# Optimization experiments

Hardware: AMD Instinct MI355X
Metric: run time of the kernel (lower is better)

The kernel has to match this reference:

```python
import jax, jax.numpy as jnp
import numpy as np

B, S, D = 4, 4096, 64

def setup_inputs() -> dict:
    key = jax.random.key(0)
    ks = jax.random.split(key, 6)
    mk = lambda k: jax.random.normal(k, (B, S, D), dtype=jnp.float32)
    return {
        "q_re": mk(ks[0]), "q_im": mk(ks[1]),
        "k_re": mk(ks[2]), "k_im": mk(ks[3]),
        "v_re": mk(ks[4]), "v_im": mk(ks[5]),
    }

def reference(q_re, q_im, k_re, k_im, v_re, v_im):
    # Complex QK^T (no conjugate, matching torch.bmm on complex tensors):
    # (qr + i qi)(kr + i ki)^T -> re = qr kr^T - qi ki^T ; im = qr ki^T + qi kr^T
    d_k = q_re.shape[-1]
    scale = 1.0 / jnp.sqrt(jnp.asarray(d_k, dtype=q_re.dtype))
    s_re = (jnp.einsum('bqd,bkd->bqk', q_re, k_re)
            - jnp.einsum('bqd,bkd->bqk', q_im, k_im)) * scale
    s_im = (jnp.einsum('bqd,bkd->bqk', q_re, k_im)
            + jnp.einsum('bqd,bkd->bqk', q_im, k_re)) * scale
    # softmax over |scores| along key axis; weights are real (imag part is 0)
    w = jax.nn.softmax(jnp.sqrt(s_re * s_re + s_im * s_im), axis=-1)  # [B,S,S]
    # CVDropout is identity in eval mode. Output = real_weights @ complex_values
    o_re = jnp.einsum('bqk,bkd->bqd', w, v_re)
    o_im = jnp.einsum('bqk,bkd->bqd', w, v_im)
    return jnp.stack([o_re, o_im], axis=0)  # [2, B, S, D] (real, imag)
```

## Files before the change

kernel.cpp:

```cpp
#include <hip/hip_runtime.h>
#include <stdint.h>

#define B_    4
#define S_    4096
#define D_    64
#define QBLK  64
#define KVBLK 64
#define NT    (S_ / KVBLK)
#define NELEM (B_ * S_ * D_)

typedef __attribute__((ext_vector_type(8))) short bf16x8;
typedef __attribute__((ext_vector_type(4))) short bf16x4;
typedef __attribute__((ext_vector_type(4))) float f32x4;
typedef __attribute__((ext_vector_type(4))) int   i32x4;
typedef __attribute__((ext_vector_type(4))) unsigned u32x4;

#define MFMA(a, b, c) __builtin_amdgcn_mfma_f32_16x16x32_bf16(a, b, c, 0, 0, 0)
#define VMWAIT(n) asm volatile("s_waitcnt vmcnt(" #n ")" ::: "memory")
#define BARRIER() do { asm volatile("" ::: "memory"); __builtin_amdgcn_s_barrier(); asm volatile("" ::: "memory"); } while (0)
#define LGKM_FENCE() do { asm volatile("s_waitcnt lgkmcnt(0)" ::: "memory"); __builtin_amdgcn_sched_barrier(0); } while (0)

__device__ __forceinline__ short f2bf(float x) {
    unsigned u = __builtin_bit_cast(unsigned, x);
    u += 0x7FFFu + ((u >> 16) & 1u);
    return (short)(u >> 16);
}

__device__ __forceinline__ unsigned cvtpk(float lo, float hi) {
    unsigned r;
    asm("v_cvt_pk_bf16_f32 %0, %1, %2" : "=v"(r) : "v"(lo), "v"(hi));
    return r;
}

__device__ __forceinline__ void async16(const short* g, short* l) {
    __builtin_amdgcn_global_load_lds(
        (const __attribute__((address_space(1))) unsigned int*)g,
        (__attribute__((address_space(3))) unsigned int*)l, 16, 0, 0);
}

__global__ __launch_bounds__(256)
void cvt4_kernel(const float* __restrict__ a0, const float* __restrict__ a1,
                 const float* __restrict__ a2, const float* __restrict__ a3,
                 short* __restrict__ ws) {
    const int idx = blockIdx.x * 256 + threadIdx.x;
    const int tn  = idx >> 18;
    const int e4  = idx & ((1 << 18) - 1);
    const float* s = (tn == 0 ? a0 : tn == 1 ? a1 : tn == 2 ? a2 : a3) + (size_t)e4 * 4;
    const float sc = (tn < 2) ? 0.125f : 1.0f;
    f32x4 x = *(const f32x4*)s;
    bf16x4 v;
#pragma unroll
    for (int c = 0; c < 4; ++c) v[c] = f2bf(x[c] * sc);
    *(bf16x4*)(ws + (size_t)tn * NELEM + (size_t)e4 * 4) = v;
}

__global__ __launch_bounds__(256)
void transpose_v_kernel(const float* __restrict__ v_re, const float* __restrict__ v_im,
                        short* __restrict__ vrT, short* __restrict__ viT) {
    __shared__ short tile[64][72];
    const int tid  = threadIdx.x;
    const int sb   = blockIdx.x;
    const int b    = blockIdx.y;
    const int comp = blockIdx.z;
    const float* src = comp ? v_im : v_re;
    short*       dst = comp ? viT : vrT;
#pragma unroll
    for (int i = 0; i < 4; ++i) {
        const int slot = i * 256 + tid;
        const int s  = slot >> 4;
        const int d4 = slot & 15;
        f32x4 x = *(const f32x4*)(src + (((size_t)b * S_) + sb * 64 + s) * D_ + d4 * 4);
#pragma unroll
        for (int c = 0; c < 4; ++c) tile[d4 * 4 + c][s] = f2bf(x[c]);
    }
    __syncthreads();
#pragma unroll
    for (int i = 0; i < 2; ++i) {
        const int slot = i * 256 + tid;
        const int d  = slot >> 3;
        const int c8 = slot & 7;
        bf16x8 v;
#pragma unroll
        for (int j = 0; j < 8; ++j) v[j] = tile[d][c8 * 8 + j];
        *(bf16x8*)(dst + ((size_t)b * 64 + d) * S_ + sb * 64 + c8 * 8) = v;
    }
}

template<int SPLIT>
__global__ __launch_bounds__(256, 4)
void cv_attn_main(const short* __restrict__ wsb,
                  float* __restrict__ out,
                  float* __restrict__ opart,
                  float* __restrict__ ml)
{
    __shared__ __align__(16) short smem[4 * KVBLK * D_];
    short* kr_s = smem;
    short* ki_s = smem + 4096;
    short* vr_s = smem + 8192;
    short* vi_s = smem + 12288;

    const int tid  = threadIdx.x;
    const int lane = tid & 63;
    const int wv   = tid >> 6;
    const int l15  = lane & 15;
    const int h    = lane >> 4;

    int bid = blockIdx.x;
    const int nwg = B_ * 64 * SPLIT;
    bid = (bid & 7) * (nwg >> 3) + (bid >> 3);
    const int qb = bid & 63;
    const int sp = (bid >> 6) % SPLIT;
    const int b  = bid / (64 * SPLIT);

    const short* qr  = wsb;
    const short* qi  = wsb + (size_t)NELEM;
    const short* kr  = wsb + 2 * (size_t)NELEM;
    const short* ki  = wsb + 3 * (size_t)NELEM;
    const short* vrT = wsb + 4 * (size_t)NELEM;
    const short* viT = wsb + 5 * (size_t)NELEM;

    const int qrow = qb * QBLK + wv * 16 + l15;
    const size_t qoff = ((size_t)b * S_ + qrow) * D_;
    bf16x8 fqr[2], fqi[2], fqn[2];
#pragma unroll
    for (int dh = 0; dh < 2; ++dh) {
        fqr[dh] = *(const bf16x8*)(qr + qoff + dh * 32 + h * 8);
        fqi[dh] = *(const bf16x8*)(qi + qoff + dh * 32 + h * 8);
        i32x4 n = __builtin_bit_cast(i32x4, fqi[dh]) ^ (int)0x80008000;
        fqn[dh] = __builtin_bit_cast(bf16x8, n);
    }

    f32x4 o_re[4], o_im[4];
#pragma unroll
    for (int i = 0; i < 4; ++i) {
        o_re[i] = (f32x4){0.f, 0.f, 0.f, 0.f};
        o_im[i] = (f32x4){0.f, 0.f, 0.f, 0.f};
    }
    float m_run = -1e30f, l_run = 0.f;
    const float L2E = 1.44269504088896f;

    const int r8   = lane >> 3;
    const int u16l = lane & 7;
    constexpr int TPB = NT / SPLIT;

    auto stageK = [&](int t) {
        const int kb = (sp * TPB + t) * KVBLK;
#pragma unroll
        for (int i = 0; i < 2; ++i) {
            const int row   = wv * 16 + i * 8 + r8;
            const int lbase = (wv * 16 + i * 8) * 64;
            const int swz   = (u16l ^ (row & 7)) << 3;
            const size_t koff = ((size_t)b * S_ + kb + row) * 64 + swz;
            async16(kr + koff, kr_s + lbase);
            async16(ki + koff, ki_s + lbase);
        }
    };
    auto stageV = [&](int t) {
        const int kb = (sp * TPB + t) * KVBLK;
#pragma unroll
        for (int i = 0; i < 2; ++i) {
            const int row   = wv * 16 + i * 8 + r8;
            const int lbase = (wv * 16 + i * 8) * 64;
            const int swz   = (u16l ^ (row & 7)) << 3;
            const size_t voff = ((size_t)b * 64 + row) * S_ + kb + swz;
            async16(vrT + voff, vr_s + lbase);
            async16(viT + voff, vi_s + lbase);
        }
    };

    stageK(0);
    stageV(0);

    for (int tt = 0; tt < TPB; ++tt) {
        const bool last = (tt == TPB - 1);

        VMWAIT(4);
        BARRIER();

        f32x4 s_re[4], s_im[4];
#pragma unroll
        for (int c = 0; c < 4; ++c) {
            s_re[c] = (f32x4){0.f, 0.f, 0.f, 0.f};
            s_im[c] = (f32x4){0.f, 0.f, 0.f, 0.f};
        }
        __builtin_amdgcn_s_setprio(1);
#pragma unroll
        for (int c = 0; c < 4; ++c) {
            const int krow = c * 16 + l15;
#pragma unroll
            for (int dh = 0; dh < 2; ++dh) {
                const int u = ((dh * 4 + h) ^ (krow & 7)) << 3;
                bf16x8 fkr = *(const bf16x8*)(kr_s + krow * 64 + u);
                bf16x8 fki = *(const bf16x8*)(ki_s + krow * 64 + u);
                s_re[c] = MFMA(fkr, fqr[dh], s_re[c]);
                s_re[c] = MFMA(fki, fqn[dh], s_re[c]);
                s_im[c] = MFMA(fki, fqr[dh], s_im[c]);
                s_im[c] = MFMA(fkr, fqi[dh], s_im[c]);
            }
        }
        __builtin_amdgcn_s_setprio(0);

        LGKM_FENCE();
        BARRIER();
        if (!last) stageK(tt + 1);

#pragma unroll
        for (int c = 0; c < 4; ++c) {
            f32x4 g = s_re[c] * s_re[c] + s_im[c] * s_im[c];
#pragma unroll
            for (int r = 0; r < 4; ++r) s_re[c][r] = __builtin_amdgcn_sqrtf(g[r]);
        }
        float tmax = s_re[0][0];
#pragma unroll
        for (int c = 0; c < 4; ++c)
#pragma unroll
            for (int r = 0; r < 4; ++r) tmax = fmaxf(tmax, s_re[c][r]);
        tmax = fmaxf(tmax, __shfl_xor(tmax, 16));
        tmax = fmaxf(tmax, __shfl_xor(tmax, 32));

        if (__any(tmax > m_run + 8.0f)) {
            const float m_new = fmaxf(m_run, tmax);
            const float alpha = __builtin_amdgcn_exp2f((m_run - m_new) * L2E);
            l_run *= alpha;
#pragma unroll
            for (int i = 0; i < 4; ++i) { o_re[i] *= alpha; o_im[i] *= alpha; }
            m_run = m_new;
        }
        const float nm = -m_run * L2E;

#pragma unroll
        for (int c = 0; c < 4; ++c)
#pragma unroll
            for (int r = 0; r < 4; ++r)
                s_im[c][r] = __builtin_amdgcn_exp2f(__builtin_fmaf(s_re[c][r], L2E, nm));
        f32x4 ps = s_im[0] + s_im[1] + s_im[2] + s_im[3];
        l_run += (ps[0] + ps[1]) + (ps[2] + ps[3]);

        bf16x8 pb[2];
#pragma unroll
        for (int hf = 0; hf < 2; ++hf) {
            u32x4 w;
            w[0] = cvtpk(s_im[hf * 2][0],     s_im[hf * 2][1]);
            w[1] = cvtpk(s_im[hf * 2][2],     s_im[hf * 2][3]);
            w[2] = cvtpk(s_im[hf * 2 + 1][0], s_im[hf * 2 + 1][1]);
            w[3] = cvtpk(s_im[hf * 2 + 1][2], s_im[hf * 2 + 1][3]);
            pb[hf] = __builtin_bit_cast(bf16x8, w);
        }

        if (!last) { VMWAIT(4); } else { VMWAIT(0); }
        BARRIER();

        __builtin_amdgcn_s_setprio(1);
#pragma unroll
        for (int hf = 0; hf < 2; ++hf) {
#pragma unroll
            for (int dc = 0; dc < 4; ++dc) {
                const int d  = dc * 16 + l15;
                const int s0 = (((hf * 4 +     (h >> 1)) ^ (l15 & 7)) << 3) + ((h & 1) << 2);
                const int s1 = (((hf * 4 + 2 + (h >> 1)) ^ (l15 & 7)) << 3) + ((h & 1) << 2);
                bf16x4 r0 = *(const bf16x4*)(vr_s + d * 64 + s0);
                bf16x4 r1 = *(const bf16x4*)(vr_s + d * 64 + s1);
                bf16x4 i0 = *(const bf16x4*)(vi_s + d * 64 + s0);
                bf16x4 i1 = *(const bf16x4*)(vi_s + d * 64 + s1);
                bf16x8 av, ai;
#pragma unroll
                for (int j = 0; j < 4; ++j) {
                    av[j] = r0[j]; av[j + 4] = r1[j];
                    ai[j] = i0[j]; ai[j + 4] = i1[j];
                }
                o_re[dc] = MFMA(av, pb[hf], o_re[dc]);
                o_im[dc] = MFMA(ai, pb[hf], o_im[dc]);
            }
        }
        __builtin_amdgcn_s_setprio(0);

        LGKM_FENCE();
        BARRIER();
        if (!last) stageV(tt + 1);
    }

    float lt = l_run;
    lt += __shfl_xor(lt, 16);
    lt += __shfl_xor(lt, 32);
    const float inv = (SPLIT == 1) ? (1.0f / lt) : 1.0f;

    float* ol = (float*)smem;

    float* dst_re;
    float* dst_im;
    if constexpr (SPLIT == 1) {
        dst_re = out + ((size_t)b * S_ + qb * QBLK) * D_;
        dst_im = dst_re + (size_t)NELEM;
    } else {
        const size_t qo = ((size_t)b * S_ + qb * QBLK) * D_;
        dst_re = opart + ((size_t)sp * 2 + 0) * NELEM + qo;
        dst_im = opart + ((size_t)sp * 2 + 1) * NELEM + qo;
    }

    auto store_comp = [&](const f32x4 (&oc)[4], float* og) {
        __syncthreads();
#pragma unroll
        for (int dc = 0; dc < 4; ++dc)
#pragma unroll
            for (int r = 0; r < 4; ++r)
                ol[(wv * 16 + l15) * 65 + dc * 16 + h * 4 + r] = oc[dc][r] * inv;
        __syncthreads();
#pragma unroll
        for (int i = 0; i < 4; ++i) {
            const int slot = i * 256 + tid;
            const int row  = slot >> 4;
            const int c4   = slot & 15;
            f32x4 v;
#pragma unroll
            for (int j = 0; j < 4; ++j) v[j] = ol[row * 65 + c4 * 4 + j];
            *(f32x4*)(og + (size_t)row * D_ + c4 * 4) = v;
        }
    };
    store_comp(o_re, dst_re);
    store_comp(o_im, dst_im);

    if constexpr (SPLIT > 1) {
        if (lane < 16) {
            const int row = qb * QBLK + wv * 16 + lane;
            const size_t mo = ((size_t)sp * (B_ * S_) + (size_t)b * S_ + row) * 2;
            ml[mo]     = m_run;
            ml[mo + 1] = lt;
        }
    }
}

template<int SPLIT>
__global__ __launch_bounds__(256)
void cv_attn_combine(const float* __restrict__ opart, const float* __restrict__ ml,
                     float* __restrict__ out) {
    const int idx  = blockIdx.x * 256 + threadIdx.x;
    const int d4   = idx & 15;
    const int rest = idx >> 4;
    const int row  = rest & (B_ * S_ - 1);
    const int comp = rest >> 14;
    float ms[SPLIT], ls[SPLIT];
    float M = -1e30f;
#pragma unroll
    for (int s = 0; s < SPLIT; ++s) {
        ms[s] = ml[((size_t)s * (B_ * S_) + row) * 2];
        ls[s] = ml[((size_t)s * (B_ * S_) + row) * 2 + 1];
        M = fmaxf(M, ms[s]);
    }
    float L = 0.f;
    f32x4 acc = (f32x4){0.f, 0.f, 0.f, 0.f};
#pragma unroll
    for (int s = 0; s < SPLIT; ++s) {
        const float w = __builtin_amdgcn_exp2f((ms[s] - M) * 1.44269504088896f);
        L += ls[s] * w;
        f32x4 o = *(const f32x4*)(opart + ((size_t)(s * 2 + comp)) * NELEM
                                  + (size_t)row * D_ + d4 * 4);
        acc += o * w;
    }
    const float invL = 1.0f / L;
    acc *= invL;
    *(f32x4*)(out + (size_t)comp * NELEM + (size_t)row * D_ + d4 * 4) = acc;
}

__global__ __launch_bounds__(256, 1)
void cv_attn_legacy(const float* __restrict__ q_re, const float* __restrict__ q_im,
                    const float* __restrict__ k_re, const float* __restrict__ k_im,
                    const float* __restrict__ v_re, const float* __restrict__ v_im,
                    float* __restrict__ out)
{
    __shared__ __align__(16) short smem[4 * KVBLK * D_];
    short* kr_s = smem;
    short* ki_s = smem + 4096;
    short* vr_s = smem + 8192;
    short* vi_s = smem + 12288;

    const int tid  = threadIdx.x;
    const int lane = tid & 63;
    const int wv   = tid >> 6;
    const int l15  = lane & 15;
    const int h    = lane >> 4;

    const int b  = blockIdx.x >> 6;
    const int qb = blockIdx.x & 63;
    const size_t boff = (size_t)b * S_ * D_;

    const int qrow = qb * QBLK + wv * 16 + l15;
    const float* qrp = q_re + boff + (size_t)qrow * D_;
    const float* qip = q_im + boff + (size_t)qrow * D_;
    bf16x8 fqr[2], fqi[2], fqn[2];
#pragma unroll
    for (int dh = 0; dh < 2; ++dh) {
        const int d0 = dh * 32 + h * 8;
        f32x4 a0 = *(const f32x4*)(qrp + d0);
        f32x4 a1 = *(const f32x4*)(qrp + d0 + 4);
        f32x4 b0 = *(const f32x4*)(qip + d0);
        f32x4 b1 = *(const f32x4*)(qip + d0 + 4);
#pragma unroll
        for (int j = 0; j < 4; ++j) {
            fqr[dh][j] = f2bf(a0[j]); fqr[dh][j + 4] = f2bf(a1[j]);
            fqi[dh][j] = f2bf(b0[j]); fqi[dh][j + 4] = f2bf(b1[j]);
            fqn[dh][j] = f2bf(-b0[j]); fqn[dh][j + 4] = f2bf(-b1[j]);
        }
    }

    f32x4 o_re[4], o_im[4];
#pragma unroll
    for (int i = 0; i < 4; ++i) {
        o_re[i] = (f32x4){0.f, 0.f, 0.f, 0.f};
        o_im[i] = (f32x4){0.f, 0.f, 0.f, 0.f};
    }
    float m_run = -1e30f, l_run = 0.f;
    const float SC = 0.125f * 1.44269504088896f;

    for (int t = 0; t < NT; ++t) {
        const int kb = t * KVBLK;
#pragma unroll
        for (int a = 0; a < 2; ++a) {
            const float* src = (a ? k_im : k_re) + boff;
            short* dst = a ? ki_s : kr_s;
#pragma unroll
            for (int i = 0; i < 2; ++i) {
                const int slot = i * 256 + tid;
                const int row  = slot >> 3;
                const int cb   = slot & 7;
                const float* p = src + (size_t)(kb + row) * D_ + cb * 8;
                f32x4 x0 = *(const f32x4*)p;
                f32x4 x1 = *(const f32x4*)(p + 4);
                bf16x8 v;
#pragma unroll
                for (int j = 0; j < 4; ++j) { v[j] = f2bf(x0[j]); v[j + 4] = f2bf(x1[j]); }
                *(bf16x8*)(dst + row * 64 + ((cb ^ (row & 7)) << 3)) = v;
            }
        }
#pragma unroll
        for (int a = 0; a < 2; ++a) {
            const float* src = (a ? v_im : v_re) + boff;
            short* dst = a ? vi_s : vr_s;
#pragma unroll
            for (int i = 0; i < 4; ++i) {
                const int slot = i * 256 + tid;
                const int k  = slot >> 4;
                const int d4 = slot & 15;
                f32x4 x = *(const f32x4*)(src + (size_t)(kb + k) * D_ + d4 * 4);
#pragma unroll
                for (int c = 0; c < 4; ++c) {
                    const int d = d4 * 4 + c;
                    dst[d * 64 + (((k >> 2) ^ (d & 15)) << 2) + (k & 3)] = f2bf(x[c]);
                }
            }
        }
        __syncthreads();

        f32x4 s_re[4], s_im[4];
#pragma unroll
        for (int c = 0; c < 4; ++c) {
            s_re[c] = (f32x4){0.f, 0.f, 0.f, 0.f};
            s_im[c] = (f32x4){0.f, 0.f, 0.f, 0.f};
        }
#pragma unroll
        for (int c = 0; c < 4; ++c) {
            const int krow = c * 16 + l15;
#pragma unroll
            for (int dh = 0; dh < 2; ++dh) {
                const int u = ((dh * 4 + h) ^ (krow & 7)) << 3;
                bf16x8 fkr = *(const bf16x8*)(kr_s + krow * 64 + u);
                bf16x8 fki = *(const bf16x8*)(ki_s + krow * 64 + u);
                s_re[c] = MFMA(fkr, fqr[dh], s_re[c]);
                s_re[c] = MFMA(fki, fqn[dh], s_re[c]);
                s_im[c] = MFMA(fki, fqr[dh], s_im[c]);
                s_im[c] = MFMA(fkr, fqi[dh], s_im[c]);
            }
        }

        float pv[4][4];
        float tmax = 0.f;
#pragma unroll
        for (int c = 0; c < 4; ++c)
#pragma unroll
            for (int r = 0; r < 4; ++r) {
                const float re = s_re[c][r], im = s_im[c][r];
                const float mg = __builtin_amdgcn_sqrtf(re * re + im * im) * SC;
                pv[c][r] = mg;
                tmax = fmaxf(tmax, mg);
            }
        tmax = fmaxf(tmax, __shfl_xor(tmax, 16));
        tmax = fmaxf(tmax, __shfl_xor(tmax, 32));
        const float m_new = fmaxf(m_run, tmax);
        const float alpha = __builtin_amdgcn_exp2f(m_run - m_new);
        m_run = m_new;
        float psum = 0.f;
#pragma unroll
        for (int c = 0; c < 4; ++c)
#pragma unroll
            for (int r = 0; r < 4; ++r) {
                const float e = __builtin_amdgcn_exp2f(pv[c][r] - m_new);
                pv[c][r] = e;
                psum += e;
            }
        l_run = l_run * alpha + psum;
#pragma unroll
        for (int i = 0; i < 4; ++i) { o_re[i] *= alpha; o_im[i] *= alpha; }

        bf16x8 pb[2];
#pragma unroll
        for (int hf = 0; hf < 2; ++hf)
#pragma unroll
            for (int j = 0; j < 4; ++j) {
                pb[hf][j]     = f2bf(pv[hf * 2][j]);
                pb[hf][j + 4] = f2bf(pv[hf * 2 + 1][j]);
            }

#pragma unroll
        for (int hf = 0; hf < 2; ++hf) {
#pragma unroll
            for (int dc = 0; dc < 4; ++dc) {
                const int d  = dc * 16 + l15;
                const int s0 = (((hf * 8) + h)     ^ l15) << 2;
                const int s1 = (((hf * 8) + 4 + h) ^ l15) << 2;
                bf16x4 r0 = *(const bf16x4*)(vr_s + d * 64 + s0);
                bf16x4 r1 = *(const bf16x4*)(vr_s + d * 64 + s1);
                bf16x4 i0 = *(const bf16x4*)(vi_s + d * 64 + s0);
                bf16x4 i1 = *(const bf16x4*)(vi_s + d * 64 + s1);
                bf16x8 av, ai;
#pragma unroll
                for (int j = 0; j < 4; ++j) {
                    av[j] = r0[j]; av[j + 4] = r1[j];
                    ai[j] = i0[j]; ai[j + 4] = i1[j];
                }
                o_re[dc] = MFMA(av, pb[hf], o_re[dc]);
                o_im[dc] = MFMA(ai, pb[hf], o_im[dc]);
            }
        }
        __syncthreads();
    }

    float lt = l_run;
    lt += __shfl_xor(lt, 16);
    lt += __shfl_xor(lt, 32);
    const float inv = 1.0f / lt;

    float* ol = (float*)smem;
    auto store_comp = [&](const f32x4 (&oc)[4], float* og) {
#pragma unroll
        for (int dc = 0; dc < 4; ++dc)
#pragma unroll
            for (int r = 0; r < 4; ++r)
                ol[(wv * 16 + l15) * 65 + dc * 16 + h * 4 + r] = oc[dc][r] * inv;
        __syncthreads();
#pragma unroll
        for (int i = 0; i < 4; ++i) {
            const int slot = i * 256 + tid;
            const int row  = slot >> 4;
            const int c4   = slot & 15;
            f32x4 v;
#pragma unroll
            for (int j = 0; j < 4; ++j) v[j] = ol[row * 65 + c4 * 4 + j];
            *(f32x4*)(og + (size_t)row * D_ + c4 * 4) = v;
        }
        __syncthreads();
    };

    float* og0 = out + boff + (size_t)(qb * QBLK) * D_;
    store_comp(o_re, og0);
    store_comp(o_im, og0 + (size_t)B_ * S_ * D_);
}

extern "C" void kernel_launch(void* const* d_in, const int* in_sizes, int n_in,
                              void* d_out, int out_size, void* d_ws, size_t ws_size,
                              hipStream_t stream) {
    (void)in_sizes; (void)n_in; (void)out_size;
    const float* q_re = (const float*)d_in[0];
    const float* q_im = (const float*)d_in[1];
    const float* k_re = (const float*)d_in[2];
    const float* k_im = (const float*)d_in[3];
    const float* v_re = (const float*)d_in[4];
    const float* v_im = (const float*)d_in[5];
    float* out = (float*)d_out;

    const size_t bf_bytes = 6 * (size_t)NELEM * 2;
    const size_t part4    = 4 * 2 * (size_t)NELEM * 4;
    const size_t ml4      = 4 * (size_t)(B_ * S_) * 2 * 4;
    const size_t need4    = bf_bytes + part4 + ml4;

    if (ws_size >= bf_bytes) {
        short* wsb = (short*)d_ws;
        cvt4_kernel<<<4096, 256, 0, stream>>>(q_re, q_im, k_re, k_im, wsb);
        transpose_v_kernel<<<dim3(64, B_, 2), 256, 0, stream>>>(
            v_re, v_im, wsb + 4 * (size_t)NELEM, wsb + 5 * (size_t)NELEM);
        if (ws_size >= need4) {
            float* opart = (float*)((char*)d_ws + bf_bytes);
            float* ml    = opart + 4 * 2 * (size_t)NELEM;
            cv_attn_main<4><<<B_ * 64 * 4, 256, 0, stream>>>(wsb, nullptr, opart, ml);
            cv_attn_combine<4><<<2048, 256, 0, stream>>>(opart, ml, out);
        } else {
            cv_attn_main<1><<<B_ * 64, 256, 0, stream>>>(wsb, out, nullptr, nullptr);
        }
    } else {
        cv_attn_legacy<<<B_ * 64, 256, 0, stream>>>(q_re, q_im, k_re, k_im, v_re, v_im, out);
    }
}
```

Measured before the change: 87.85 us.

## Merge prepass kernels, permute V layout for vector LDS reads, raise KV split to 8

```diff
diff --git a/kernel.cpp b/kernel.cpp
--- a/kernel.cpp
+++ b/kernel.cpp
@@ -8,12 +8,14 @@
 #define KVBLK 64
 #define NT    (S_ / KVBLK)
 #define NELEM (B_ * S_ * D_)
+#define BS_   (B_ * S_)
 
 typedef __attribute__((ext_vector_type(8))) short bf16x8;
 typedef __attribute__((ext_vector_type(4))) short bf16x4;
 typedef __attribute__((ext_vector_type(4))) float f32x4;
 typedef __attribute__((ext_vector_type(4))) int   i32x4;
 typedef __attribute__((ext_vector_type(4))) unsigned u32x4;
+typedef __attribute__((ext_vector_type(4))) _Float16 f16x4;
 
 #define MFMA(a, b, c) __builtin_amdgcn_mfma_f32_16x16x32_bf16(a, b, c, 0, 0, 0)
 #define VMWAIT(n) asm volatile("s_waitcnt vmcnt(" #n ")" ::: "memory")
@@ -39,58 +41,62 @@
 }
 
 __global__ __launch_bounds__(256)
-void cvt4_kernel(const float* __restrict__ a0, const float* __restrict__ a1,
-                 const float* __restrict__ a2, const float* __restrict__ a3,
-                 short* __restrict__ ws) {
-    const int idx = blockIdx.x * 256 + threadIdx.x;
-    const int tn  = idx >> 18;
-    const int e4  = idx & ((1 << 18) - 1);
-    const float* s = (tn == 0 ? a0 : tn == 1 ? a1 : tn == 2 ? a2 : a3) + (size_t)e4 * 4;
-    const float sc = (tn < 2) ? 0.125f : 1.0f;
-    f32x4 x = *(const f32x4*)s;
-    bf16x4 v;
-#pragma unroll
-    for (int c = 0; c < 4; ++c) v[c] = f2bf(x[c] * sc);
-    *(bf16x4*)(ws + (size_t)tn * NELEM + (size_t)e4 * 4) = v;
-}
-
-__global__ __launch_bounds__(256)
-void transpose_v_kernel(const float* __restrict__ v_re, const float* __restrict__ v_im,
-                        short* __restrict__ vrT, short* __restrict__ viT) {
-    __shared__ short tile[64][72];
+void prepass_kernel(const float* __restrict__ q_re, const float* __restrict__ q_im,
+                    const float* __restrict__ k_re, const float* __restrict__ k_im,
+                    const float* __restrict__ v_re, const float* __restrict__ v_im,
+                    short* __restrict__ ws) {
+    const int bidx = blockIdx.x;
     const int tid  = threadIdx.x;
-    const int sb   = blockIdx.x;
-    const int b    = blockIdx.y;
-    const int comp = blockIdx.z;
-    const float* src = comp ? v_im : v_re;
-    short*       dst = comp ? viT : vrT;
-#pragma unroll
-    for (int i = 0; i < 4; ++i) {
-        const int slot = i * 256 + tid;
-        const int s  = slot >> 4;
-        const int d4 = slot & 15;
-        f32x4 x = *(const f32x4*)(src + (((size_t)b * S_) + sb * 64 + s) * D_ + d4 * 4);
-#pragma unroll
-        for (int c = 0; c < 4; ++c) tile[d4 * 4 + c][s] = f2bf(x[c]);
-    }
-    __syncthreads();
-#pragma unroll
-    for (int i = 0; i < 2; ++i) {
-        const int slot = i * 256 + tid;
-        const int d  = slot >> 3;
-        const int c8 = slot & 7;
-        bf16x8 v;
-#pragma unroll
-        for (int j = 0; j < 8; ++j) v[j] = tile[d][c8 * 8 + j];
-        *(bf16x8*)(dst + ((size_t)b * 64 + d) * S_ + sb * 64 + c8 * 8) = v;
-    }
-}
-
-template<int SPLIT>
+    if (bidx < 4096) {
+        const int idx = bidx * 256 + tid;
+        const int tn  = idx >> 18;
+        const int e4  = idx & ((1 << 18) - 1);
+        const float* s = (tn == 0 ? q_re : tn == 1 ? q_im : tn == 2 ? k_re : k_im)
+                         + (size_t)e4 * 4;
+        const float sc = (tn < 2) ? 0.125f : 1.0f;
+        f32x4 x = *(const f32x4*)s;
+        bf16x4 v;
+#pragma unroll
+        for (int c = 0; c < 4; ++c) v[c] = f2bf(x[c] * sc);
+        *(bf16x4*)(ws + (size_t)tn * NELEM + (size_t)e4 * 4) = v;
+    } else {
+        __shared__ short tile[64][72];
+        const int tb   = bidx - 4096;
+        const int sb   = tb & 63;
+        const int b    = (tb >> 6) & 3;
+        const int comp = tb >> 8;
+        const float* src = comp ? v_im : v_re;
+        short* dst = ws + (size_t)(4 + comp) * NELEM;
+#pragma unroll
+        for (int i = 0; i < 4; ++i) {
+            const int slot = i * 256 + tid;
+            const int s  = slot >> 4;
+            const int d4 = slot & 15;
+            f32x4 x = *(const f32x4*)(src + (((size_t)b * S_) + sb * 64 + s) * D_ + d4 * 4);
+#pragma unroll
+            for (int c = 0; c < 4; ++c) tile[d4 * 4 + c][s] = f2bf(x[c]);
+        }
+        __syncthreads();
+#pragma unroll
+        for (int i = 0; i < 2; ++i) {
+            const int slot = i * 256 + tid;
+            const int d = slot >> 3;
+            const int m = slot & 7;
+            const int a = m >> 2, hh = m & 3;
+            bf16x8 v;
+#pragma unroll
+            for (int j = 0; j < 8; ++j)
+                v[j] = tile[d][a * 32 + hh * 4 + ((j >> 2) << 4) + (j & 3)];
+            *(bf16x8*)(dst + ((size_t)b * 64 + d) * S_ + sb * 64 + m * 8) = v;
+        }
+    }
+}
+
+template<int SPLIT, typename OT>
 __global__ __launch_bounds__(256, 4)
 void cv_attn_main(const short* __restrict__ wsb,
                   float* __restrict__ out,
-                  float* __restrict__ opart,
+                  OT* __restrict__ opart,
                   float* __restrict__ ml)
 {
     __shared__ __align__(16) short smem[4 * KVBLK * D_];
@@ -119,6 +125,9 @@
     const short* vrT = wsb + 4 * (size_t)NELEM;
     const short* viT = wsb + 5 * (size_t)NELEM;
 
+    short* kb0 = smem + l15 * 64 + ((h ^ (l15 & 7)) << 3);
+    short* kb1 = smem + l15 * 64 + (((h ^ 4) ^ (l15 & 7)) << 3);
+
     const int qrow = qb * QBLK + wv * 16 + l15;
     const size_t qoff = ((size_t)b * S_ + qrow) * D_;
     bf16x8 fqr[2], fqi[2], fqn[2];
@@ -186,17 +195,18 @@
         __builtin_amdgcn_s_setprio(1);
 #pragma unroll
         for (int c = 0; c < 4; ++c) {
-            const int krow = c * 16 + l15;
-#pragma unroll
-            for (int dh = 0; dh < 2; ++dh) {
-                const int u = ((dh * 4 + h) ^ (krow & 7)) << 3;
-                bf16x8 fkr = *(const bf16x8*)(kr_s + krow * 64 + u);
-                bf16x8 fki = *(const bf16x8*)(ki_s + krow * 64 + u);
-                s_re[c] = MFMA(fkr, fqr[dh], s_re[c]);
-                s_re[c] = MFMA(fki, fqn[dh], s_re[c]);
-                s_im[c] = MFMA(fki, fqr[dh], s_im[c]);
-                s_im[c] = MFMA(fkr, fqi[dh], s_im[c]);
-            }
+            bf16x8 fkr0 = *(const bf16x8*)(kb0 + c * 1024);
+            bf16x8 fkr1 = *(const bf16x8*)(kb1 + c * 1024);
+            bf16x8 fki0 = *(const bf16x8*)(kb0 + 4096 + c * 1024);
+            bf16x8 fki1 = *(const bf16x8*)(kb1 + 4096 + c * 1024);
+            s_re[c] = MFMA(fkr0, fqr[0], s_re[c]);
+            s_re[c] = MFMA(fkr1, fqr[1], s_re[c]);
+            s_re[c] = MFMA(fki0, fqn[0], s_re[c]);
+            s_re[c] = MFMA(fki1, fqn[1], s_re[c]);
+            s_im[c] = MFMA(fki0, fqr[0], s_im[c]);
+            s_im[c] = MFMA(fki1, fqr[1], s_im[c]);
+            s_im[c] = MFMA(fkr0, fqi[0], s_im[c]);
+            s_im[c] = MFMA(fkr1, fqi[1], s_im[c]);
         }
         __builtin_amdgcn_s_setprio(0);
 
@@ -253,21 +263,11 @@
         __builtin_amdgcn_s_setprio(1);
 #pragma unroll
         for (int hf = 0; hf < 2; ++hf) {
+            const short* kbh = hf ? kb1 : kb0;
 #pragma unroll
             for (int dc = 0; dc < 4; ++dc) {
-                const int d  = dc * 16 + l15;
-                const int s0 = (((hf * 4 +     (h >> 1)) ^ (l15 & 7)) << 3) + ((h & 1) << 2);
-                const int s1 = (((hf * 4 + 2 + (h >> 1)) ^ (l15 & 7)) << 3) + ((h & 1) << 2);
-                bf16x4 r0 = *(const bf16x4*)(vr_s + d * 64 + s0);
-                bf16x4 r1 = *(const bf16x4*)(vr_s + d * 64 + s1);
-                bf16x4 i0 = *(const bf16x4*)(vi_s + d * 64 + s0);
-                bf16x4 i1 = *(const bf16x4*)(vi_s + d * 64 + s1);
-                bf16x8 av, ai;
-#pragma unroll
-                for (int j = 0; j < 4; ++j) {
-                    av[j] = r0[j]; av[j + 4] = r1[j];
-                    ai[j] = i0[j]; ai[j + 4] = i1[j];
-                }
+                bf16x8 av = *(const bf16x8*)(kbh + 8192  + dc * 1024);
+                bf16x8 ai = *(const bf16x8*)(kbh + 12288 + dc * 1024);
                 o_re[dc] = MFMA(av, pb[hf], o_re[dc]);
                 o_im[dc] = MFMA(ai, pb[hf], o_im[dc]);
             }
@@ -286,10 +286,10 @@
 
     float* ol = (float*)smem;
 
-    float* dst_re;
-    float* dst_im;
+    OT* dst_re;
+    OT* dst_im;
     if constexpr (SPLIT == 1) {
-        dst_re = out + ((size_t)b * S_ + qb * QBLK) * D_;
+        dst_re = (OT*)out + ((size_t)b * S_ + qb * QBLK) * D_;
         dst_im = dst_re + (size_t)NELEM;
     } else {
         const size_t qo = ((size_t)b * S_ + qb * QBLK) * D_;
@@ -297,7 +297,7 @@
         dst_im = opart + ((size_t)sp * 2 + 1) * NELEM + qo;
     }
 
-    auto store_comp = [&](const f32x4 (&oc)[4], float* og) {
+    auto store_comp = [&](const f32x4 (&oc)[4], OT* og) {
         __syncthreads();
 #pragma unroll
         for (int dc = 0; dc < 4; ++dc)
@@ -313,7 +313,14 @@
             f32x4 v;
 #pragma unroll
             for (int j = 0; j < 4; ++j) v[j] = ol[row * 65 + c4 * 4 + j];
-            *(f32x4*)(og + (size_t)row * D_ + c4 * 4) = v;
+            if constexpr (sizeof(OT) == 4) {
+                *(f32x4*)((float*)og + (size_t)row * D_ + c4 * 4) = v;
+            } else {
+                f16x4 hv;
+#pragma unroll
+                for (int j = 0; j < 4; ++j) hv[j] = (_Float16)v[j];
+                *(f16x4*)((_Float16*)og + (size_t)row * D_ + c4 * 4) = hv;
+            }
         }
     };
     store_comp(o_re, dst_re);
@@ -322,28 +329,28 @@
     if constexpr (SPLIT > 1) {
         if (lane < 16) {
             const int row = qb * QBLK + wv * 16 + lane;
-            const size_t mo = ((size_t)sp * (B_ * S_) + (size_t)b * S_ + row) * 2;
+            const size_t mo = ((size_t)sp * BS_ + (size_t)b * S_ + row) * 2;
             ml[mo]     = m_run;
             ml[mo + 1] = lt;
         }
     }
 }
 
-template<int SPLIT>
+template<int SPLIT, typename OT>
 __global__ __launch_bounds__(256)
-void cv_attn_combine(const float* __restrict__ opart, const float* __restrict__ ml,
+void cv_attn_combine(const OT* __restrict__ opart, const float* __restrict__ ml,
                      float* __restrict__ out) {
     const int idx  = blockIdx.x * 256 + threadIdx.x;
     const int d4   = idx & 15;
     const int rest = idx >> 4;
-    const int row  = rest & (B_ * S_ - 1);
+    const int row  = rest & (BS_ - 1);
     const int comp = rest >> 14;
     float ms[SPLIT], ls[SPLIT];
     float M = -1e30f;
 #pragma unroll
     for (int s = 0; s < SPLIT; ++s) {
-        ms[s] = ml[((size_t)s * (B_ * S_) + row) * 2];
-        ls[s] = ml[((size_t)s * (B_ * S_) + row) * 2 + 1];
+        ms[s] = ml[((size_t)s * BS_ + row) * 2];
+        ls[s] = ml[((size_t)s * BS_ + row) * 2 + 1];
         M = fmaxf(M, ms[s]);
     }
     float L = 0.f;
@@ -352,8 +359,15 @@
     for (int s = 0; s < SPLIT; ++s) {
         const float w = __builtin_amdgcn_exp2f((ms[s] - M) * 1.44269504088896f);
         L += ls[s] * w;
-        f32x4 o = *(const f32x4*)(opart + ((size_t)(s * 2 + comp)) * NELEM
-                                  + (size_t)row * D_ + d4 * 4);
+        const OT* op = opart + ((size_t)(s * 2 + comp)) * NELEM + (size_t)row * D_ + d4 * 4;
+        f32x4 o;
+        if constexpr (sizeof(OT) == 4) {
+            o = *(const f32x4*)op;
+        } else {
+            f16x4 hv = *(const f16x4*)op;
+#pragma unroll
+            for (int j = 0; j < 4; ++j) o[j] = (float)hv[j];
+        }
         acc += o * w;
     }
     const float invL = 1.0f / L;
@@ -577,22 +591,31 @@
     float* out = (float*)d_out;
 
     const size_t bf_bytes = 6 * (size_t)NELEM * 2;
-    const size_t part4    = 4 * 2 * (size_t)NELEM * 4;
-    const size_t ml4      = 4 * (size_t)(B_ * S_) * 2 * 4;
-    const size_t need4    = bf_bytes + part4 + ml4;
+    const size_t need8f32 = bf_bytes + 8 * 2 * (size_t)NELEM * 4 + 8 * (size_t)BS_ * 8;
+    const size_t need8f16 = bf_bytes + 8 * 2 * (size_t)NELEM * 2 + 8 * (size_t)BS_ * 8;
+    const size_t need4f32 = bf_bytes + 4 * 2 * (size_t)NELEM * 4 + 4 * (size_t)BS_ * 8;
 
     if (ws_size >= bf_bytes) {
         short* wsb = (short*)d_ws;
-        cvt4_kernel<<<4096, 256, 0, stream>>>(q_re, q_im, k_re, k_im, wsb);
-        transpose_v_kernel<<<dim3(64, B_, 2), 256, 0, stream>>>(
-            v_re, v_im, wsb + 4 * (size_t)NELEM, wsb + 5 * (size_t)NELEM);
-        if (ws_size >= need4) {
-            float* opart = (float*)((char*)d_ws + bf_bytes);
-            float* ml    = opart + 4 * 2 * (size_t)NELEM;
-            cv_attn_main<4><<<B_ * 64 * 4, 256, 0, stream>>>(wsb, nullptr, opart, ml);
-            cv_attn_combine<4><<<2048, 256, 0, stream>>>(opart, ml, out);
+        prepass_kernel<<<4608, 256, 0, stream>>>(q_re, q_im, k_re, k_im, v_re, v_im, wsb);
+        char* extra = (char*)d_ws + bf_bytes;
+        if (ws_size >= need8f32) {
+            float* opart = (float*)extra;
+            float* ml    = (float*)(extra + 8 * 2 * (size_t)NELEM * 4);
+            cv_attn_main<8, float><<<B_ * 64 * 8, 256, 0, stream>>>(wsb, nullptr, opart, ml);
+            cv_attn_combine<8, float><<<2048, 256, 0, stream>>>(opart, ml, out);
+        } else if (ws_size >= need8f16) {
+            _Float16* opart = (_Float16*)extra;
+            float* ml = (float*)(extra + 8 * 2 * (size_t)NELEM * 2);
+            cv_attn_main<8, _Float16><<<B_ * 64 * 8, 256, 0, stream>>>(wsb, nullptr, opart, ml);
+            cv_attn_combine<8, _Float16><<<2048, 256, 0, stream>>>(opart, ml, out);
+        } else if (ws_size >= need4f32) {
+            float* opart = (float*)extra;
+            float* ml    = (float*)(extra + 4 * 2 * (size_t)NELEM * 4);
+            cv_attn_main<4, float><<<B_ * 64 * 4, 256, 0, stream>>>(wsb, nullptr, opart, ml);
+            cv_attn_combine<4, float><<<2048, 256, 0, stream>>>(opart, ml, out);
         } else {
-            cv_attn_main<1><<<B_ * 64, 256, 0, stream>>>(wsb, out, nullptr, nullptr);
+            cv_attn_main<1, float><<<B_ * 64, 256, 0, stream>>>(wsb, out, out, nullptr);
         }
     } else {
         cv_attn_legacy<<<B_ * 64, 256, 0, stream>>>(q_re, q_im, k_re, k_im, v_re, v_im, out);
```

After: 88.41 us. Within noise of the previous version (+0.6%).
